# Performance work log

Measured on AMD Instinct MI355X. Metric: run time of the kernel, lower is better.

Reference implementation:

```python
import jax, jax.numpy as jnp
import numpy as np
import math

H = 8
C = 512
HIDE = 2048
LN_EPS = 1e-6


def setup_inputs() -> dict:
    key = jax.random.key(0)
    ks = jax.random.split(key, 9)
    B, N = 4, 2048
    std = 0.02
    return {
        "q": jax.random.normal(ks[0], (B, N, C), jnp.float32),
        "k": jax.random.normal(ks[1], (B, N, C), jnp.float32),
        "v": jax.random.normal(ks[2], (B, N, C), jnp.float32),
        "fc1_w": jax.random.normal(ks[3], (HIDE, C), jnp.float32) * std,
        "fc1_b": jnp.zeros((HIDE,), jnp.float32),
        "fc2_w": jax.random.normal(ks[4], (C, HIDE), jnp.float32) * std,
        "fc2_b": jnp.zeros((C,), jnp.float32),
        "ln1_w": jnp.ones((C,), jnp.float32),
        "ln1_b": jnp.zeros((C,), jnp.float32),
        "ln2_w": jnp.ones((C,), jnp.float32),
        "ln2_b": jnp.zeros((C,), jnp.float32),
    }


def _layernorm(x, w, b):
    mu = jnp.mean(x, axis=-1, keepdims=True)
    var = jnp.var(x, axis=-1, keepdims=True)
    return (x - mu) * jax.lax.rsqrt(var + LN_EPS) * w + b


def _mha(q, k, v):
    B, N, _ = q.shape
    hd = C // H
    # [B, H, N, hd]
    qh = q.reshape(B, N, H, hd).transpose(0, 2, 1, 3)
    kh = k.reshape(B, N, H, hd).transpose(0, 2, 1, 3)
    vh = v.reshape(B, N, H, hd).transpose(0, 2, 1, 3)
    scores = jnp.einsum('bhqd,bhkd->bhqk', qh, kh) / math.sqrt(hd)
    probs = jax.nn.softmax(scores, axis=-1)
    out = jnp.einsum('bhqk,bhkd->bhqd', probs, vh)
    return out.transpose(0, 2, 1, 3).reshape(B, N, C)


def reference(q, k, v, fc1_w, fc1_b, fc2_w, fc2_b, ln1_w, ln1_b, ln2_w, ln2_b):
    attn = _mha(q, k, v)
    q2 = _layernorm(q + attn, ln1_w, ln1_b)
    h = jax.nn.gelu(q2 @ fc1_w.T + fc1_b, approximate=False)
    mlp = h @ fc2_w.T + fc2_b
    return _layernorm(q2 + mlp, ln2_w, ln2_b)
```

## Files before the change

kernel.cpp:

```cpp
#include <hip/hip_runtime.h>
#include <math.h>

typedef unsigned short u16;
typedef __bf16 bf16_t;
typedef bf16_t bf16x4 __attribute__((ext_vector_type(4)));
typedef bf16_t bf16x8 __attribute__((ext_vector_type(8)));
typedef short s16x4 __attribute__((ext_vector_type(4)));
typedef float f32x4 __attribute__((ext_vector_type(4)));

typedef const __attribute__((address_space(1))) void* gcp;
typedef __attribute__((address_space(3))) void* lcp;

#define BB 4
#define NN 2048
#define CC 512
#define HH 8
#define HD 64
#define HIDE_ 2048
#define TT (BB*NN)

#if __has_builtin(__builtin_amdgcn_exp2f)
#define EXP2(x) __builtin_amdgcn_exp2f(x)
#else
#define EXP2(x) __expf((x) * 0.69314718055994531f)
#endif

#if __has_builtin(__builtin_amdgcn_rcpf)
#define RCP(x) __builtin_amdgcn_rcpf(x)
#else
#define RCP(x) (1.0f / (x))
#endif

__device__ __forceinline__ u16 f2bf(float f) {
  unsigned u = __float_as_uint(f);
  u += 0x7FFF + ((u >> 16) & 1);
  return (u16)(u >> 16);
}

__device__ __forceinline__ int xcd_swz(int orig, int nwg) {
  return (orig & 7) * (nwg >> 3) + (orig >> 3);
}

__device__ __forceinline__ void bf8_to_f(const u16* p, float* f) {
  uint4 u = *(const uint4*)p;
  f[0] = __uint_as_float(u.x << 16); f[1] = __uint_as_float(u.x & 0xffff0000u);
  f[2] = __uint_as_float(u.y << 16); f[3] = __uint_as_float(u.y & 0xffff0000u);
  f[4] = __uint_as_float(u.z << 16); f[5] = __uint_as_float(u.z & 0xffff0000u);
  f[6] = __uint_as_float(u.w << 16); f[7] = __uint_as_float(u.w & 0xffff0000u);
}

__device__ __forceinline__ bf16x8 ldq8(const float* p, float s) {
  float4 a = *(const float4*)p;
  float4 b = *(const float4*)(p + 4);
  bf16x8 r = {(bf16_t)(a.x * s), (bf16_t)(a.y * s), (bf16_t)(a.z * s), (bf16_t)(a.w * s),
              (bf16_t)(b.x * s), (bf16_t)(b.y * s), (bf16_t)(b.z * s), (bf16_t)(b.w * s)};
  return r;
}

__device__ __forceinline__ float gelu_tanh(float x) {
  float y = 0.7978845608028654f * x * (1.0f + 0.044715f * x * x);
  float a = y * 2.8853900817779268f;
  a = fminf(fmaxf(a, -30.0f), 30.0f);
  float e = EXP2(a);
  float t = (e - 1.0f) * RCP(e + 1.0f);
  return 0.5f * x * (1.0f + t);
}

__global__ __launch_bounds__(256) void prep_kernel(const float* __restrict__ k,
                                                   const float* __restrict__ fc1w,
                                                   const float* __restrict__ fc2w,
                                                   const float* __restrict__ v,
                                                   u16* __restrict__ kb,
                                                   u16* __restrict__ w1b,
                                                   u16* __restrict__ w2b,
                                                   u16* __restrict__ vtb) {
  __shared__ __align__(16) u16 T[64 * 72];
  int bid = blockIdx.x, tid = threadIdx.x;
  if (bid < 3072) {
    const float* in;
    u16* out;
    int rel;
    if (bid < 2048)      { in = k;    out = kb;  rel = bid; }
    else if (bid < 2560) { in = fc1w; out = w1b; rel = bid - 2048; }
    else                 { in = fc2w; out = w2b; rel = bid - 2560; }
    int i = (rel * 256 + tid) * 8;
    float4 a = *(const float4*)(in + i);
    float4 b2 = *(const float4*)(in + i + 4);
    u16 r[8] = {f2bf(a.x), f2bf(a.y), f2bf(a.z), f2bf(a.w),
                f2bf(b2.x), f2bf(b2.y), f2bf(b2.z), f2bf(b2.w)};
    *(uint4*)(out + i) = *(const uint4*)r;
    return;
  }
  int tv = bid - 3072;
  int j0 = (tv & 31) * 64;
  int bh = tv >> 5;
  int b = bh >> 3, h = bh & 7;
#pragma unroll
  for (int i = 0; i < 4; i++) {
    int idx = i * 256 + tid;
    int j = idx >> 4, dq = idx & 15;
    float4 a = *(const float4*)(v + ((size_t)(b * NN + j0 + j)) * CC + h * 64 + dq * 4);
    T[(dq * 4 + 0) * 72 + j] = f2bf(a.x);
    T[(dq * 4 + 1) * 72 + j] = f2bf(a.y);
    T[(dq * 4 + 2) * 72 + j] = f2bf(a.z);
    T[(dq * 4 + 3) * 72 + j] = f2bf(a.w);
  }
  __syncthreads();
#pragma unroll
  for (int i = 0; i < 2; i++) {
    int idx = i * 256 + tid;
    int d = idx >> 3, jb = idx & 7;
    uint4 val = *(const uint4*)&T[d * 72 + jb * 8];
    *(uint4*)&vtb[((size_t)(bh * 64 + d)) * NN + j0 + jb * 8] = val;
  }
}

__global__ __launch_bounds__(256, 4) void attn_kernel(const float* __restrict__ qf,
                                                      const u16* __restrict__ kb,
                                                      const u16* __restrict__ vtb,
                                                      u16* __restrict__ ou,
                                                      float* __restrict__ lsum,
                                                      float qs) {
  __shared__ __align__(16) u16 Ks[64 * 64];
  __shared__ __align__(16) u16 Vs[64 * 64];
  int tid = threadIdx.x, wave = tid >> 6, lane = tid & 63;
  int l15 = lane & 15, quad = lane >> 4;
  int r7 = l15 & 7;
  int bid = xcd_swz(blockIdx.x, 512);
  int half = blockIdx.y;
  int qt = bid & 15, h = (bid >> 4) & 7, b = bid >> 7;
  int qw = qt * 128 + wave * 32;
  int j0base = half * 1024;

  u16* ou_ = ou + (size_t)half * TT * CC;
  float* ls_ = lsum + (size_t)half * TT * HH;

  const float* qp = qf + ((size_t)(b * NN + qw + l15)) * CC + h * 64 + quad * 8;
  bf16x8 qfA0 = ldq8(qp, qs);
  bf16x8 qfA1 = ldq8(qp + 32, qs);
  bf16x8 qfB0 = ldq8(qp + (size_t)16 * CC, qs);
  bf16x8 qfB1 = ldq8(qp + (size_t)16 * CC + 32, qs);

  int rl = lane >> 3;
  int cb = (lane & 7) ^ rl;
  int rK = wave * 16 + rl;
  size_t vtbase = ((size_t)(b * HH + h)) * 64 * NN;
  const u16* kp0 = kb + ((size_t)(b * NN + j0base + rK)) * CC + h * 64 + cb * 8;
  const u16* kp1 = kp0 + (size_t)8 * CC;
  const u16* vp0 = vtb + vtbase + (size_t)rK * NN + j0base + cb * 8;
  const u16* vp1 = vp0 + (size_t)8 * NN;
  lcp lK0 = (lcp)&Ks[wave * 16 * 64];
  lcp lK1 = (lcp)&Ks[wave * 16 * 64 + 8 * 64];
  lcp lV0 = (lcp)&Vs[wave * 16 * 64];
  lcp lV1 = (lcp)&Vs[wave * 16 * 64 + 8 * 64];

  float lA = 0.f, lB = 0.f;
  f32x4 oA[4] = {}, oB[4] = {};

  for (int kt = 0; kt < 16; kt++) {
    __syncthreads();
    __builtin_amdgcn_global_load_lds((gcp)kp0, lK0, 16, 0, 0);
    __builtin_amdgcn_global_load_lds((gcp)kp1, lK1, 16, 0, 0);
    __builtin_amdgcn_global_load_lds((gcp)vp0, lV0, 16, 0, 0);
    __builtin_amdgcn_global_load_lds((gcp)vp1, lV1, 16, 0, 0);
    kp0 += (size_t)64 * CC; kp1 += (size_t)64 * CC;
    vp0 += 64; vp1 += 64;
    __syncthreads();

    s16x4 pfA[4], pfB[4];
    __builtin_amdgcn_s_setprio(1);
#pragma unroll
    for (int nt = 0; nt < 4; nt++) {
      const u16* krow = &Ks[(nt * 16 + l15) * 64];
      bf16x8 k0 = *(const bf16x8*)&krow[(quad ^ r7) * 8];
      bf16x8 k1 = *(const bf16x8*)&krow[((quad + 4) ^ r7) * 8];
      f32x4 zA = {0.f, 0.f, 0.f, 0.f}, zB = {0.f, 0.f, 0.f, 0.f};
      zA = __builtin_amdgcn_mfma_f32_16x16x32_bf16(k0, qfA0, zA, 0, 0, 0);
      zA = __builtin_amdgcn_mfma_f32_16x16x32_bf16(k1, qfA1, zA, 0, 0, 0);
      zB = __builtin_amdgcn_mfma_f32_16x16x32_bf16(k0, qfB0, zB, 0, 0, 0);
      zB = __builtin_amdgcn_mfma_f32_16x16x32_bf16(k1, qfB1, zB, 0, 0, 0);
      float a0 = EXP2(zA[0]), a1 = EXP2(zA[1]), a2 = EXP2(zA[2]), a3 = EXP2(zA[3]);
      float b0 = EXP2(zB[0]), b1 = EXP2(zB[1]), b2 = EXP2(zB[2]), b3 = EXP2(zB[3]);
      lA += (a0 + a1) + (a2 + a3);
      lB += (b0 + b1) + (b2 + b3);
      bf16x4 ta = {(bf16_t)a0, (bf16_t)a1, (bf16_t)a2, (bf16_t)a3};
      bf16x4 tb = {(bf16_t)b0, (bf16_t)b1, (bf16_t)b2, (bf16_t)b3};
      pfA[nt] = __builtin_bit_cast(s16x4, ta);
      pfB[nt] = __builtin_bit_cast(s16x4, tb);
    }
#pragma unroll
    for (int dt = 0; dt < 4; dt++) {
      const u16* vrow = &Vs[(dt * 16 + l15) * 64];
#pragma unroll
      for (int nt = 0; nt < 4; nt++) {
        s16x4 vf = *(const s16x4*)
            &vrow[((nt * 2 + (quad >> 1)) ^ r7) * 8 + (quad & 1) * 4];
        oA[dt] = __builtin_amdgcn_mfma_f32_16x16x16bf16_1k(vf, pfA[nt], oA[dt], 0, 0, 0);
        oB[dt] = __builtin_amdgcn_mfma_f32_16x16x16bf16_1k(vf, pfB[nt], oB[dt], 0, 0, 0);
      }
    }
    __builtin_amdgcn_s_setprio(0);
  }

  lA += __shfl_xor(lA, 16, 64);
  lA += __shfl_xor(lA, 32, 64);
  lB += __shfl_xor(lB, 16, 64);
  lB += __shfl_xor(lB, 32, 64);
  if (quad == 0) {
    ls_[(size_t)(b * NN + qw + l15) * HH + h] = lA;
    ls_[(size_t)(b * NN + qw + 16 + l15) * HH + h] = lB;
  }
  size_t obase = ((size_t)(b * NN + qw + l15)) * CC + h * 64 + quad * 4;
#pragma unroll
  for (int dt = 0; dt < 4; dt++) {
    u16 ra[4] = {f2bf(oA[dt][0]), f2bf(oA[dt][1]), f2bf(oA[dt][2]), f2bf(oA[dt][3])};
    u16 rb[4] = {f2bf(oB[dt][0]), f2bf(oB[dt][1]), f2bf(oB[dt][2]), f2bf(oB[dt][3])};
    *(uint2*)&ou_[obase + dt * 16] = *(const uint2*)ra;
    *(uint2*)&ou_[obase + (size_t)16 * CC + dt * 16] = *(const uint2*)rb;
  }
}

__global__ __launch_bounds__(256) void ln1_kernel(const float* __restrict__ q,
                                                  const u16* __restrict__ ou,
                                                  const float* __restrict__ lsum,
                                                  const float* __restrict__ w,
                                                  const float* __restrict__ bb,
                                                  u16* __restrict__ outb) {
  int tid = threadIdx.x;
  int row = blockIdx.x * 4 + (tid >> 6);
  int lane = tid & 63;
  int h = lane >> 3;
  size_t base = (size_t)row * CC + lane * 8;
  const u16* ou1 = ou + (size_t)TT * CC;
  const float* ls1 = lsum + (size_t)TT * HH;
  float li = lsum[(size_t)row * HH + h] + ls1[(size_t)row * HH + h];
  float inv = 1.0f / li;
  float4 a0 = *(const float4*)(q + base);
  float4 a1 = *(const float4*)(q + base + 4);
  float c[8], d[8];
  bf8_to_f(ou + base, c);
  bf8_to_f(ou1 + base, d);
  float av[8] = {a0.x, a0.y, a0.z, a0.w, a1.x, a1.y, a1.z, a1.w};
  float x[8];
#pragma unroll
  for (int i = 0; i < 8; i++) x[i] = av[i] + (c[i] + d[i]) * inv;
  float sum = 0.f, sq = 0.f;
#pragma unroll
  for (int i = 0; i < 8; i++) { sum += x[i]; sq += x[i] * x[i]; }
#pragma unroll
  for (int msk = 1; msk < 64; msk <<= 1) {
    sum += __shfl_xor(sum, msk, 64);
    sq += __shfl_xor(sq, msk, 64);
  }
  float mu = sum * (1.0f / CC);
  float var = sq * (1.0f / CC) - mu * mu;
  float rs = rsqrtf(var + 1e-6f);
  int col = lane * 8;
  float4 w0 = *(const float4*)(w + col);
  float4 w1 = *(const float4*)(w + col + 4);
  float4 b0 = *(const float4*)(bb + col);
  float4 b1 = *(const float4*)(bb + col + 4);
  float wv[8] = {w0.x, w0.y, w0.z, w0.w, w1.x, w1.y, w1.z, w1.w};
  float bv[8] = {b0.x, b0.y, b0.z, b0.w, b1.x, b1.y, b1.z, b1.w};
  u16 r[8];
#pragma unroll
  for (int i = 0; i < 8; i++) r[i] = f2bf((x[i] - mu) * rs * wv[i] + bv[i]);
  *(uint4*)(outb + base) = *(const uint4*)r;
}

__global__ __launch_bounds__(256) void ln2_kernel(const u16* __restrict__ q2b,
                                                  const u16* __restrict__ mp,
                                                  const float* __restrict__ fb,
                                                  const float* __restrict__ w,
                                                  const float* __restrict__ bb,
                                                  float* __restrict__ outf) {
  int tid = threadIdx.x;
  int row = blockIdx.x * 4 + (tid >> 6);
  int lane = tid & 63;
  size_t base = (size_t)row * CC + lane * 8;
  const u16* mp1 = mp + (size_t)TT * CC;
  int col = lane * 8;
  float a[8], c[8], d[8];
  bf8_to_f(q2b + base, a);
  bf8_to_f(mp + base, c);
  bf8_to_f(mp1 + base, d);
  float4 f0 = *(const float4*)(fb + col);
  float4 f1 = *(const float4*)(fb + col + 4);
  float fbv[8] = {f0.x, f0.y, f0.z, f0.w, f1.x, f1.y, f1.z, f1.w};
  float x[8];
#pragma unroll
  for (int i = 0; i < 8; i++) x[i] = a[i] + (c[i] + d[i]) + fbv[i];
  float sum = 0.f, sq = 0.f;
#pragma unroll
  for (int i = 0; i < 8; i++) { sum += x[i]; sq += x[i] * x[i]; }
#pragma unroll
  for (int msk = 1; msk < 64; msk <<= 1) {
    sum += __shfl_xor(sum, msk, 64);
    sq += __shfl_xor(sq, msk, 64);
  }
  float mu = sum * (1.0f / CC);
  float var = sq * (1.0f / CC) - mu * mu;
  float rs = rsqrtf(var + 1e-6f);
  float4 w0 = *(const float4*)(w + col);
  float4 w1 = *(const float4*)(w + col + 4);
  float4 b0 = *(const float4*)(bb + col);
  float4 b1 = *(const float4*)(bb + col + 4);
  float wv[8] = {w0.x, w0.y, w0.z, w0.w, w1.x, w1.y, w1.z, w1.w};
  float bv[8] = {b0.x, b0.y, b0.z, b0.w, b1.x, b1.y, b1.z, b1.w};
  float y[8];
#pragma unroll
  for (int i = 0; i < 8; i++) y[i] = (x[i] - mu) * rs * wv[i] + bv[i];
  *(float4*)(outf + base) = make_float4(y[0], y[1], y[2], y[3]);
  *(float4*)(outf + base + 4) = make_float4(y[4], y[5], y[6], y[7]);
}

template <bool GELU>
__global__ __launch_bounds__(256) void gemm128(const u16* __restrict__ A,
                                               const u16* __restrict__ Bw,
                                               const float* __restrict__ bias,
                                               u16* __restrict__ outb,
                                               int Nn, int K, int NT,
                                               int gx, int gy) {
  __shared__ __align__(16) u16 As[2][128 * 64];
  __shared__ __align__(16) u16 Bs[2][128 * 64];
  int tid = threadIdx.x, wave = tid >> 6, lane = tid & 63;
  int l15 = lane & 15, quad = lane >> 4;
  int r7 = l15 & 7;
  int l = xcd_swz(blockIdx.x, gridDim.x);
  int bx = l % gx;
  int by = (l / gx) % gy;
  int bz = l / (gx * gy);
  int m0 = by * 128, n0 = bx * 128;
  int kbeg = bz * (NT * 64);
  u16* outz = outb + (size_t)bz * ((size_t)TT * CC);
  int wm = (wave >> 1) * 64, wn = (wave & 1) * 64;
  int w32 = wave * 32;
  int rl = lane >> 3;
  int cb = (lane & 7) ^ rl;
  const u16* Ap = &A[(size_t)(m0 + w32 + rl) * K + kbeg + cb * 8];
  const u16* Bp = &Bw[(size_t)(n0 + w32 + rl) * K + kbeg + cb * 8];
  unsigned sb = w32 * 64;

  f32x4 acc[4][4] = {};

  auto stage = [&](int buf, int kofs) {
#pragma unroll
    for (int c = 0; c < 4; c++) {
      __builtin_amdgcn_global_load_lds((gcp)(Ap + kofs + (size_t)(c * 8) * K),
          (lcp)&As[buf][sb + c * 512], 16, 0, 0);
      __builtin_amdgcn_global_load_lds((gcp)(Bp + kofs + (size_t)(c * 8) * K),
          (lcp)&Bs[buf][sb + c * 512], 16, 0, 0);
    }
  };

  stage(0, 0);
  stage(1, 64);
  asm volatile("s_waitcnt vmcnt(8)" ::: "memory");
  __builtin_amdgcn_s_barrier();

  for (int t = 0; t < NT; t++) {
    int buf = t & 1;
    bool pf = (t + 2) < NT;
    bf16x8 aF[4][2], bF[4][2];
#pragma unroll
    for (int m = 0; m < 4; m++)
#pragma unroll
      for (int kh = 0; kh < 2; kh++)
        aF[m][kh] = *(const bf16x8*)&As[buf][(wm + m * 16 + l15) * 64 +
                                            ((kh * 4 + quad) ^ r7) * 8];
#pragma unroll
    for (int n = 0; n < 4; n++)
#pragma unroll
      for (int kh = 0; kh < 2; kh++)
        bF[n][kh] = *(const bf16x8*)&Bs[buf][(wn + n * 16 + l15) * 64 +
                                            ((kh * 4 + quad) ^ r7) * 8];
    __builtin_amdgcn_s_setprio(1);
#pragma unroll
    for (int m = 0; m < 4; m++)
#pragma unroll
      for (int n = 0; n < 2; n++)
#pragma unroll
        for (int kh = 0; kh < 2; kh++)
          acc[m][n] = __builtin_amdgcn_mfma_f32_16x16x32_bf16(aF[m][kh], bF[n][kh],
                                                              acc[m][n], 0, 0, 0);
    __builtin_amdgcn_s_setprio(0);
    asm volatile("s_waitcnt lgkmcnt(0)\n\ts_barrier" ::: "memory");
    if (pf) stage(buf, (t + 2) * 64);
    __builtin_amdgcn_s_setprio(1);
#pragma unroll
    for (int m = 0; m < 4; m++)
#pragma unroll
      for (int n = 2; n < 4; n++)
#pragma unroll
        for (int kh = 0; kh < 2; kh++)
          acc[m][n] = __builtin_amdgcn_mfma_f32_16x16x32_bf16(aF[m][kh], bF[n][kh],
                                                              acc[m][n], 0, 0, 0);
    __builtin_amdgcn_s_setprio(0);
    if (t + 1 < NT) {
      if (pf) asm volatile("s_waitcnt vmcnt(8)" ::: "memory");
      else    asm volatile("s_waitcnt vmcnt(0)" ::: "memory");
      __builtin_amdgcn_s_barrier();
      asm volatile("" ::: "memory");
    }
  }

#pragma unroll
  for (int am = 0; am < 4; am++)
#pragma unroll
    for (int bn = 0; bn < 4; bn++) {
      int rowi = m0 + wm + am * 16 + quad * 4;
      int col = n0 + wn + bn * 16 + l15;
      float bcol = GELU ? bias[col] : 0.0f;
#pragma unroll
      for (int r = 0; r < 4; r++) {
        float val = acc[am][bn][r] + bcol;
        if (GELU) val = gelu_tanh(val);
        outz[(size_t)(rowi + r) * Nn + col] = f2bf(val);
      }
    }
}

extern "C" void kernel_launch(void* const* d_in, const int* in_sizes, int n_in,
                              void* d_out, int out_size, void* d_ws, size_t ws_size,
                              hipStream_t stream) {
  const float* q = (const float*)d_in[0];
  const float* k = (const float*)d_in[1];
  const float* v = (const float*)d_in[2];
  const float* fc1_w = (const float*)d_in[3];
  const float* fc1_b = (const float*)d_in[4];
  const float* fc2_w = (const float*)d_in[5];
  const float* fc2_b = (const float*)d_in[6];
  const float* ln1_w = (const float*)d_in[7];
  const float* ln1_b = (const float*)d_in[8];
  const float* ln2_w = (const float*)d_in[9];
  const float* ln2_b = (const float*)d_in[10];
  float* out = (float*)d_out;

  char* ws = (char*)d_ws;
  size_t off = 0;
  u16* kb = (u16*)(ws + off); off += (size_t)TT * CC * 2;
  u16* vtb = (u16*)(ws + off); off += (size_t)TT * CC * 2;
  u16* w1b = (u16*)(ws + off); off += (size_t)HIDE_ * CC * 2;
  u16* w2b = (u16*)(ws + off); off += (size_t)CC * HIDE_ * 2;
  u16* ou = (u16*)(ws + off); off += (size_t)2 * TT * CC * 2;
  float* lsum = (float*)(ws + off); off += (size_t)2 * TT * HH * 4;
  u16* q2b = (u16*)(ws + off); off += (size_t)TT * CC * 2;
  u16* hbuf = (u16*)(ws + off); off += (size_t)TT * HIDE_ * 2;
  u16* mp = (u16*)(ws + off); off += (size_t)2 * TT * CC * 2;

  const float QS = 0.18033688011112042f;
  prep_kernel<<<4096, 256, 0, stream>>>(k, fc1_w, fc2_w, v, kb, w1b, w2b, vtb);
  attn_kernel<<<dim3(512, 2), 256, 0, stream>>>(q, kb, vtb, ou, lsum, QS);
  ln1_kernel<<<2048, 256, 0, stream>>>(q, ou, lsum, ln1_w, ln1_b, q2b);
  gemm128<true><<<1024, 256, 0, stream>>>(q2b, w1b, fc1_b, hbuf, HIDE_, CC, 8, 16, 64);
  gemm128<false><<<512, 256, 0, stream>>>(hbuf, w2b, fc2_b, mp, CC, HIDE_, 16, 4, 64);
  ln2_kernel<<<2048, 256, 0, stream>>>(q2b, mp, fc2_b, ln2_w, ln2_b, out);
}
```

Measured before the change: 219.2 us.

## Move weight conversion into attention tail blocks and stage GEMM epilogue through LDS

The fc1/fc2 weight fp32→bf16 conversion moves out of the prep kernel into 1024 extra blocks appended to the attention grid. Those blocks run in the attention kernel's tail and may hide under it. The attention grid is flattened to 1D, with the half index taken from the block id. The GEMM epilogue now writes bf16 results into a padded LDS tile in two passes, then stores coalesced 8-byte chunks instead of scattered 2-byte global stores, at the cost of extra barriers.

```diff
diff --git a/kernel.cpp b/kernel.cpp
--- a/kernel.cpp
+++ b/kernel.cpp
@@ -67,31 +67,21 @@
 }
 
 __global__ __launch_bounds__(256) void prep_kernel(const float* __restrict__ k,
-                                                   const float* __restrict__ fc1w,
-                                                   const float* __restrict__ fc2w,
                                                    const float* __restrict__ v,
                                                    u16* __restrict__ kb,
-                                                   u16* __restrict__ w1b,
-                                                   u16* __restrict__ w2b,
                                                    u16* __restrict__ vtb) {
   __shared__ __align__(16) u16 T[64 * 72];
   int bid = blockIdx.x, tid = threadIdx.x;
-  if (bid < 3072) {
-    const float* in;
-    u16* out;
-    int rel;
-    if (bid < 2048)      { in = k;    out = kb;  rel = bid; }
-    else if (bid < 2560) { in = fc1w; out = w1b; rel = bid - 2048; }
-    else                 { in = fc2w; out = w2b; rel = bid - 2560; }
-    int i = (rel * 256 + tid) * 8;
-    float4 a = *(const float4*)(in + i);
-    float4 b2 = *(const float4*)(in + i + 4);
+  if (bid < 2048) {
+    int i = (bid * 256 + tid) * 8;
+    float4 a = *(const float4*)(k + i);
+    float4 b2 = *(const float4*)(k + i + 4);
     u16 r[8] = {f2bf(a.x), f2bf(a.y), f2bf(a.z), f2bf(a.w),
                 f2bf(b2.x), f2bf(b2.y), f2bf(b2.z), f2bf(b2.w)};
-    *(uint4*)(out + i) = *(const uint4*)r;
+    *(uint4*)(kb + i) = *(const uint4*)r;
     return;
   }
-  int tv = bid - 3072;
+  int tv = bid - 2048;
   int j0 = (tv & 31) * 64;
   int bh = tv >> 5;
   int b = bh >> 3, h = bh & 7;
@@ -118,16 +108,35 @@
 __global__ __launch_bounds__(256, 4) void attn_kernel(const float* __restrict__ qf,
                                                       const u16* __restrict__ kb,
                                                       const u16* __restrict__ vtb,
+                                                      const float* __restrict__ fc1w,
+                                                      const float* __restrict__ fc2w,
+                                                      u16* __restrict__ w1b,
+                                                      u16* __restrict__ w2b,
                                                       u16* __restrict__ ou,
                                                       float* __restrict__ lsum,
                                                       float qs) {
   __shared__ __align__(16) u16 Ks[64 * 64];
   __shared__ __align__(16) u16 Vs[64 * 64];
-  int tid = threadIdx.x, wave = tid >> 6, lane = tid & 63;
+  int raw = blockIdx.x;
+  int tid = threadIdx.x;
+  if (raw >= 1024) {
+    int cid = raw - 1024;
+    const float* in = (cid < 512) ? fc1w : fc2w;
+    u16* outp = (cid < 512) ? w1b : w2b;
+    int rel = cid & 511;
+    int i = (rel * 256 + tid) * 8;
+    float4 a = *(const float4*)(in + i);
+    float4 b2 = *(const float4*)(in + i + 4);
+    u16 r[8] = {f2bf(a.x), f2bf(a.y), f2bf(a.z), f2bf(a.w),
+                f2bf(b2.x), f2bf(b2.y), f2bf(b2.z), f2bf(b2.w)};
+    *(uint4*)(outp + i) = *(const uint4*)r;
+    return;
+  }
+  int wave = tid >> 6, lane = tid & 63;
   int l15 = lane & 15, quad = lane >> 4;
-  int r7 = l15 & 7;
-  int bid = xcd_swz(blockIdx.x, 512);
-  int half = blockIdx.y;
+  int r7 = lane & 7; r7 = l15 & 7;
+  int half = raw >> 9;
+  int bid = xcd_swz(raw & 511, 512);
   int qt = bid & 15, h = (bid >> 4) & 7, b = bid >> 7;
   int qw = qt * 128 + wave * 32;
   int j0base = half * 1024;
@@ -321,8 +330,7 @@
                                                u16* __restrict__ outb,
                                                int Nn, int K, int NT,
                                                int gx, int gy) {
-  __shared__ __align__(16) u16 As[2][128 * 64];
-  __shared__ __align__(16) u16 Bs[2][128 * 64];
+  __shared__ __align__(16) u16 SH[32768];
   int tid = threadIdx.x, wave = tid >> 6, lane = tid & 63;
   int l15 = lane & 15, quad = lane >> 4;
   int r7 = l15 & 7;
@@ -347,9 +355,9 @@
 #pragma unroll
     for (int c = 0; c < 4; c++) {
       __builtin_amdgcn_global_load_lds((gcp)(Ap + kofs + (size_t)(c * 8) * K),
-          (lcp)&As[buf][sb + c * 512], 16, 0, 0);
+          (lcp)&SH[buf * 8192 + sb + c * 512], 16, 0, 0);
       __builtin_amdgcn_global_load_lds((gcp)(Bp + kofs + (size_t)(c * 8) * K),
-          (lcp)&Bs[buf][sb + c * 512], 16, 0, 0);
+          (lcp)&SH[16384 + buf * 8192 + sb + c * 512], 16, 0, 0);
     }
   };
 
@@ -366,14 +374,14 @@
     for (int m = 0; m < 4; m++)
 #pragma unroll
       for (int kh = 0; kh < 2; kh++)
-        aF[m][kh] = *(const bf16x8*)&As[buf][(wm + m * 16 + l15) * 64 +
-                                            ((kh * 4 + quad) ^ r7) * 8];
+        aF[m][kh] = *(const bf16x8*)&SH[buf * 8192 + (wm + m * 16 + l15) * 64 +
+                                        ((kh * 4 + quad) ^ r7) * 8];
 #pragma unroll
     for (int n = 0; n < 4; n++)
 #pragma unroll
       for (int kh = 0; kh < 2; kh++)
-        bF[n][kh] = *(const bf16x8*)&Bs[buf][(wn + n * 16 + l15) * 64 +
-                                            ((kh * 4 + quad) ^ r7) * 8];
+        bF[n][kh] = *(const bf16x8*)&SH[16384 + buf * 8192 + (wn + n * 16 + l15) * 64 +
+                                        ((kh * 4 + quad) ^ r7) * 8];
     __builtin_amdgcn_s_setprio(1);
 #pragma unroll
     for (int m = 0; m < 4; m++)
@@ -404,20 +412,35 @@
     }
   }
 
-#pragma unroll
-  for (int am = 0; am < 4; am++)
-#pragma unroll
-    for (int bn = 0; bn < 4; bn++) {
-      int rowi = m0 + wm + am * 16 + quad * 4;
-      int col = n0 + wn + bn * 16 + l15;
-      float bcol = GELU ? bias[col] : 0.0f;
-#pragma unroll
-      for (int r = 0; r < 4; r++) {
-        float val = acc[am][bn][r] + bcol;
-        if (GELU) val = gelu_tanh(val);
-        outz[(size_t)(rowi + r) * Nn + col] = f2bf(val);
-      }
-    }
+  const int PIT = 140;
+#pragma unroll
+  for (int p = 0; p < 2; p++) {
+    __syncthreads();
+    if ((wave >> 1) == p) {
+#pragma unroll
+      for (int am = 0; am < 4; am++)
+#pragma unroll
+        for (int bn = 0; bn < 4; bn++) {
+          int colg = n0 + wn + bn * 16 + l15;
+          float bcol = GELU ? bias[colg] : 0.0f;
+#pragma unroll
+          for (int r = 0; r < 4; r++) {
+            float val = acc[am][bn][r] + bcol;
+            if (GELU) val = gelu_tanh(val);
+            SH[(am * 16 + quad * 4 + r) * PIT + wn + bn * 16 + l15] = f2bf(val);
+          }
+        }
+    }
+    __syncthreads();
+#pragma unroll
+    for (int i = 0; i < 8; i++) {
+      int idx = i * 256 + tid;
+      int r = idx >> 5;
+      int c4 = idx & 31;
+      uint2 vv = *(const uint2*)&SH[r * PIT + c4 * 4];
+      *(uint2*)&outz[(size_t)(m0 + p * 64 + r) * Nn + n0 + c4 * 4] = vv;
+    }
+  }
 }
 
 extern "C" void kernel_launch(void* const* d_in, const int* in_sizes, int n_in,
@@ -449,8 +472,9 @@
   u16* mp = (u16*)(ws + off); off += (size_t)2 * TT * CC * 2;
 
   const float QS = 0.18033688011112042f;
-  prep_kernel<<<4096, 256, 0, stream>>>(k, fc1_w, fc2_w, v, kb, w1b, w2b, vtb);
-  attn_kernel<<<dim3(512, 2), 256, 0, stream>>>(q, kb, vtb, ou, lsum, QS);
+  prep_kernel<<<3072, 256, 0, stream>>>(k, v, kb, vtb);
+  attn_kernel<<<2048, 256, 0, stream>>>(q, kb, vtb, fc1_w, fc2_w, w1b, w2b,
+                                        ou, lsum, QS);
   ln1_kernel<<<2048, 256, 0, stream>>>(q, ou, lsum, ln1_w, ln1_b, q2b);
   gemm128<true><<<1024, 256, 0, stream>>>(q2b, w1b, fc1_b, hbuf, HIDE_, CC, 8, 16, 64);
   gemm128<false><<<512, 256, 0, stream>>>(hbuf, w2b, fc2_b, mp, CC, HIDE_, 16, 4, 64);
```

Result: slower. 227.8 us (+3.9%).

## Remove split-KV in attention and normalize output in-kernel

Applied to the files above, without the earlier changes.

Attention now processes the full key range per block instead of splitting it into two halves over a second grid dimension. It normalizes by the row sum before writing a single bf16 output. This removes the duplicated partial-output buffer, the lsum buffer, and the combine work in ln1. In exchange the grid is halved, reducing parallelism and occupancy for the attention kernel.

```diff
diff --git a/kernel.cpp b/kernel.cpp
--- a/kernel.cpp
+++ b/kernel.cpp
@@ -119,7 +119,6 @@
                                                       const u16* __restrict__ kb,
                                                       const u16* __restrict__ vtb,
                                                       u16* __restrict__ ou,
-                                                      float* __restrict__ lsum,
                                                       float qs) {
   __shared__ __align__(16) u16 Ks[64 * 64];
   __shared__ __align__(16) u16 Vs[64 * 64];
@@ -127,13 +126,8 @@
   int l15 = lane & 15, quad = lane >> 4;
   int r7 = l15 & 7;
   int bid = xcd_swz(blockIdx.x, 512);
-  int half = blockIdx.y;
   int qt = bid & 15, h = (bid >> 4) & 7, b = bid >> 7;
   int qw = qt * 128 + wave * 32;
-  int j0base = half * 1024;
-
-  u16* ou_ = ou + (size_t)half * TT * CC;
-  float* ls_ = lsum + (size_t)half * TT * HH;
 
   const float* qp = qf + ((size_t)(b * NN + qw + l15)) * CC + h * 64 + quad * 8;
   bf16x8 qfA0 = ldq8(qp, qs);
@@ -145,9 +139,9 @@
   int cb = (lane & 7) ^ rl;
   int rK = wave * 16 + rl;
   size_t vtbase = ((size_t)(b * HH + h)) * 64 * NN;
-  const u16* kp0 = kb + ((size_t)(b * NN + j0base + rK)) * CC + h * 64 + cb * 8;
+  const u16* kp0 = kb + ((size_t)(b * NN + rK)) * CC + h * 64 + cb * 8;
   const u16* kp1 = kp0 + (size_t)8 * CC;
-  const u16* vp0 = vtb + vtbase + (size_t)rK * NN + j0base + cb * 8;
+  const u16* vp0 = vtb + vtbase + (size_t)rK * NN + cb * 8;
   const u16* vp1 = vp0 + (size_t)8 * NN;
   lcp lK0 = (lcp)&Ks[wave * 16 * 64];
   lcp lK1 = (lcp)&Ks[wave * 16 * 64 + 8 * 64];
@@ -157,7 +151,7 @@
   float lA = 0.f, lB = 0.f;
   f32x4 oA[4] = {}, oB[4] = {};
 
-  for (int kt = 0; kt < 16; kt++) {
+  for (int kt = 0; kt < 32; kt++) {
     __syncthreads();
     __builtin_amdgcn_global_load_lds((gcp)kp0, lK0, 16, 0, 0);
     __builtin_amdgcn_global_load_lds((gcp)kp1, lK1, 16, 0, 0);
@@ -206,44 +200,37 @@
   lA += __shfl_xor(lA, 32, 64);
   lB += __shfl_xor(lB, 16, 64);
   lB += __shfl_xor(lB, 32, 64);
-  if (quad == 0) {
-    ls_[(size_t)(b * NN + qw + l15) * HH + h] = lA;
-    ls_[(size_t)(b * NN + qw + 16 + l15) * HH + h] = lB;
-  }
+  float invA = 1.0f / lA;
+  float invB = 1.0f / lB;
   size_t obase = ((size_t)(b * NN + qw + l15)) * CC + h * 64 + quad * 4;
 #pragma unroll
   for (int dt = 0; dt < 4; dt++) {
-    u16 ra[4] = {f2bf(oA[dt][0]), f2bf(oA[dt][1]), f2bf(oA[dt][2]), f2bf(oA[dt][3])};
-    u16 rb[4] = {f2bf(oB[dt][0]), f2bf(oB[dt][1]), f2bf(oB[dt][2]), f2bf(oB[dt][3])};
-    *(uint2*)&ou_[obase + dt * 16] = *(const uint2*)ra;
-    *(uint2*)&ou_[obase + (size_t)16 * CC + dt * 16] = *(const uint2*)rb;
+    u16 ra[4] = {f2bf(oA[dt][0] * invA), f2bf(oA[dt][1] * invA),
+                 f2bf(oA[dt][2] * invA), f2bf(oA[dt][3] * invA)};
+    u16 rb[4] = {f2bf(oB[dt][0] * invB), f2bf(oB[dt][1] * invB),
+                 f2bf(oB[dt][2] * invB), f2bf(oB[dt][3] * invB)};
+    *(uint2*)&ou[obase + dt * 16] = *(const uint2*)ra;
+    *(uint2*)&ou[obase + (size_t)16 * CC + dt * 16] = *(const uint2*)rb;
   }
 }
 
 __global__ __launch_bounds__(256) void ln1_kernel(const float* __restrict__ q,
                                                   const u16* __restrict__ ou,
-                                                  const float* __restrict__ lsum,
                                                   const float* __restrict__ w,
                                                   const float* __restrict__ bb,
                                                   u16* __restrict__ outb) {
   int tid = threadIdx.x;
   int row = blockIdx.x * 4 + (tid >> 6);
   int lane = tid & 63;
-  int h = lane >> 3;
   size_t base = (size_t)row * CC + lane * 8;
-  const u16* ou1 = ou + (size_t)TT * CC;
-  const float* ls1 = lsum + (size_t)TT * HH;
-  float li = lsum[(size_t)row * HH + h] + ls1[(size_t)row * HH + h];
-  float inv = 1.0f / li;
   float4 a0 = *(const float4*)(q + base);
   float4 a1 = *(const float4*)(q + base + 4);
-  float c[8], d[8];
+  float c[8];
   bf8_to_f(ou + base, c);
-  bf8_to_f(ou1 + base, d);
   float av[8] = {a0.x, a0.y, a0.z, a0.w, a1.x, a1.y, a1.z, a1.w};
   float x[8];
 #pragma unroll
-  for (int i = 0; i < 8; i++) x[i] = av[i] + (c[i] + d[i]) * inv;
+  for (int i = 0; i < 8; i++) x[i] = av[i] + c[i];
   float sum = 0.f, sq = 0.f;
 #pragma unroll
   for (int i = 0; i < 8; i++) { sum += x[i]; sq += x[i] * x[i]; }
@@ -442,16 +429,15 @@
   u16* vtb = (u16*)(ws + off); off += (size_t)TT * CC * 2;
   u16* w1b = (u16*)(ws + off); off += (size_t)HIDE_ * CC * 2;
   u16* w2b = (u16*)(ws + off); off += (size_t)CC * HIDE_ * 2;
-  u16* ou = (u16*)(ws + off); off += (size_t)2 * TT * CC * 2;
-  float* lsum = (float*)(ws + off); off += (size_t)2 * TT * HH * 4;
+  u16* ou = (u16*)(ws + off); off += (size_t)TT * CC * 2;
   u16* q2b = (u16*)(ws + off); off += (size_t)TT * CC * 2;
   u16* hbuf = (u16*)(ws + off); off += (size_t)TT * HIDE_ * 2;
   u16* mp = (u16*)(ws + off); off += (size_t)2 * TT * CC * 2;
 
   const float QS = 0.18033688011112042f;
   prep_kernel<<<4096, 256, 0, stream>>>(k, fc1_w, fc2_w, v, kb, w1b, w2b, vtb);
-  attn_kernel<<<dim3(512, 2), 256, 0, stream>>>(q, kb, vtb, ou, lsum, QS);
-  ln1_kernel<<<2048, 256, 0, stream>>>(q, ou, lsum, ln1_w, ln1_b, q2b);
+  attn_kernel<<<512, 256, 0, stream>>>(q, kb, vtb, ou, QS);
+  ln1_kernel<<<2048, 256, 0, stream>>>(q, ou, ln1_w, ln1_b, q2b);
   gemm128<true><<<1024, 256, 0, stream>>>(q2b, w1b, fc1_b, hbuf, HIDE_, CC, 8, 16, 64);
   gemm128<false><<<512, 256, 0, stream>>>(hbuf, w2b, fc2_b, mp, CC, HIDE_, 16, 4, 64);
   ln2_kernel<<<2048, 256, 0, stream>>>(q2b, mp, fc2_b, ln2_w, ln2_b, out);
```

Result: no change. 220.7 us, median of 2 (+0.7%).
